# Kernel optimization log

Measured on AMD Instinct MI355X. Metric: run time of the kernel, lower is better.

The kernel has to match this reference:

```python
import jax, jax.numpy as jnp
import numpy as np

SR = 22050.0  # samplerate; nyquist = SR/2


def _conv1d(x, w, b, pad):
    # x: [B, Cin, T], w: [Cout, Cin, K]
    y = jax.lax.conv_general_dilated(x, w, (1,), [(pad, pad)],
                                     dimension_numbers=('NCH', 'OIH', 'NCH'))
    return y + b[None, :, None]


def _lrelu(x):
    return jnp.where(x >= 0, x, 0.2 * x)


def _lin_upsample(x, factor):
    # torch F.upsample(mode='linear', align_corners=False) ~ half-pixel linear resize
    B, C, T = x.shape
    return jax.image.resize(x, (B, C, T * factor), method='linear')


def _oscillator_bank(f, a, sr):
    # f, a: [B, n_osc, T] -> audio [B, T]
    f = jnp.clip(f, 20.0, sr / 2.0)
    phase = jnp.cumsum(f * (2.0 * np.pi / sr), axis=-1)  # cumulative phase integration
    return jnp.sum(jnp.sin(phase) * a, axis=1)


def _noise_bank2(mags, noise):
    # mags: [B, n_coeffs, n_frames] rfft magnitudes per frame; noise: [B, total_samples]
    B, n_coeffs, n_frames = mags.shape
    window = (n_coeffs - 1) * 2
    hop = window // 2
    total = hop * n_frames
    padded = jnp.pad(noise, ((0, 0), (0, hop)))           # [B, total + hop]
    blocks = padded.reshape(B, n_frames + 1, hop)
    frames = jnp.concatenate([blocks[:, :-1], blocks[:, 1:]], axis=-1)  # [B, n_frames, window]
    spec = jnp.fft.rfft(frames, axis=-1)                   # [B, n_frames, n_coeffs]
    spec = spec * mags.transpose(0, 2, 1)                  # filter white noise per frame
    filt = jnp.fft.irfft(spec, n=window, axis=-1)          # (torch normalized rfft/irfft scales cancel)
    out = jnp.zeros((B, hop * (n_frames + 1)), filt.dtype)
    out = out.at[:, :n_frames * hop].add(filt[..., :hop].reshape(B, -1))
    out = out.at[:, hop:].add(filt[..., hop:].reshape(B, -1))
    return out[:, :total].reshape(B, 1, total)


def _forward(x, noise, mw0, mb0, mw1, mb1, mw2, mb2, mw3, mb3, fw, fb,
             gw0, gb0, gw1, gb1, gw2, gb2, gw3, gb3, lw, lb,
             nw0, nb0, nw1, nb1, nw2, nb2, nw3, nb3, nlw, nlb):
    B, _, T = x.shape
    up = noise.shape[1] // T  # upsample_factor = output_size // input_size
    n_osc = fw.shape[0]

    # oscillator frequency ranges (constants, as in __init__)
    stops = np.geomspace(20.0, SR / 2.0, num=n_osc)
    diffs = np.diff(np.concatenate([[0.0], stops]))
    starts = jnp.asarray(stops - diffs, jnp.float32)[None, :, None]
    diffs_j = jnp.asarray(diffs, jnp.float32)[None, :, None]

    # loudness path (main2 -> loudness ** 2)
    h = x
    for w_, b_ in ((gw0, gb0), (gw1, gb1), (gw2, gb2), (gw3, gb3)):
        h = _lrelu(_conv1d(h, w_, b_, 1))
    loud = _conv1d(h, lw, lb, 1) ** 2  # [B, n_osc, T]

    # frequency path (main -> sigmoid -> map to [start, stop])
    h = x
    for w_, b_ in ((mw0, mb0), (mw1, mb1), (mw2, mb2), (mw3, mb3)):
        h = _lrelu(_conv1d(h, w_, b_, 1))
    f = starts + jax.nn.sigmoid(_conv1d(h, fw, fb, 1)) * diffs_j  # [B, n_osc, T]

    h = x
    for w_, b_ in ((nw0, nb0), (nw1, nb1), (nw2, nb2), (nw3, nb3)):
        h = jnp.repeat(h, 2, axis=-1)
        h = _lrelu(_conv1d(h, w_, b_, 3))
    n_l = _conv1d(h, nlw, nlb, 1) ** 2  # [B, 17, 1024]

    loud = _lin_upsample(loud, up)  # [B, n_osc, output_size]
    f = _lin_upsample(f, up)
    harmonic = _oscillator_bank(f, loud, SR).reshape(B, 1, -1)
    return harmonic + _noise_bank2(n_l, noise)


def setup_inputs() -> dict:
    key = jax.random.key(0)
    ks = jax.random.split(key, 40)
    B, Cin, T, c, n_osc, out_size = 16, 128, 64, 512, 128, 16384
    n_coeffs = out_size // 1024 + 1  # 17
    inp = {}
    inp['x'] = jax.random.normal(ks[0], (B, Cin, T), jnp.float32)
    inp['noise'] = jax.random.uniform(ks[1], (B, out_size), jnp.float32, minval=-1.0, maxval=1.0)
    specs = [('mw0', c, Cin, 3), ('mw1', c, c, 3), ('mw2', c, c, 3), ('mw3', c, c, 3), ('fw', n_osc, c, 3),
             ('gw0', c, Cin, 3), ('gw1', c, c, 3), ('gw2', c, c, 3), ('gw3', c, c, 3), ('lw', n_osc, c, 3),
             ('nw0', c, Cin, 7), ('nw1', c, c, 7), ('nw2', c, c, 7), ('nw3', c, c, 7), ('nlw', n_coeffs, c, 3)]
    for j, (nm, o, i, ksz) in enumerate(specs):
        kw, kb = jax.random.split(ks[2 + j])
        inp[nm] = jax.random.normal(kw, (o, i, ksz), jnp.float32) * (1.0 / np.sqrt(i * ksz))
        inp[nm.replace('w', 'b', 1)] = jax.random.normal(kb, (o,), jnp.float32) * 0.01
    return inp


def reference(x, noise, mw0, mb0, mw1, mb1, mw2, mb2, mw3, mb3, fw, fb,
              gw0, gb0, gw1, gb1, gw2, gb2, gw3, gb3, lw, lb,
              nw0, nb0, nw1, nb1, nw2, nb2, nw3, nb3, nlw, nlb):
    return _forward(x, noise, mw0, mb0, mw1, mb1, mw2, mb2, mw3, mb3, fw, fb,
                    gw0, gb0, gw1, gb1, gw2, gb2, gw3, gb3, lw, lb,
                    nw0, nb0, nw1, nb1, nw2, nb2, nw3, nb3, nlw, nlb)
```

## Files before the change

kernel.cpp:

```cpp
#include <hip/hip_runtime.h>
#include <math.h>

#define ACT_LRELU  0
#define ACT_SIGMAP 1
#define ACT_SQUARE 2

typedef __attribute__((ext_vector_type(8))) short v8s;
typedef __attribute__((ext_vector_type(4))) short v4s;
typedef __attribute__((ext_vector_type(16))) float f32x16;

static __device__ __forceinline__ float lrelu(float x) { return x >= 0.f ? x : 0.2f * x; }

static __device__ __forceinline__ short bf16rne(float x) {
  unsigned u = __float_as_uint(x);
  unsigned r = (u + 0x7FFFu + ((u >> 16) & 1u)) >> 16;
  return (short)r;
}
static __device__ __forceinline__ float bf16tof(short h) {
  return __uint_as_float(((unsigned)(unsigned short)h) << 16);
}
static __device__ __forceinline__ void split3(float v, short& h, short& l, short& q) {
  h = bf16rne(v); float r1 = v - bf16tof(h);
  l = bf16rne(r1); float r2 = r1 - bf16tof(l);
  q = bf16rne(r2);
}

__global__ void __launch_bounds__(256) prep_acts(
    const float* __restrict__ x, short* __restrict__ xm3)
{
  int e = blockIdx.x * 256 + threadIdx.x;
  if (e >= 131072) return;
  int b = e >> 13, rem = e & 8191, t = rem >> 7, ci = rem & 127;
  float v = x[((size_t)(b * 128) + ci) * 64 + t];
  short h, l, q; split3(v, h, l, q);
  size_t o = ((size_t)(b * 64) + t) * 128 + ci;
  xm3[0 * 131072 + o] = h;
  xm3[1 * 131072 + o] = l;
  xm3[2 * 131072 + o] = q;
}

__global__ void __launch_bounds__(256) prep_panels(
    const float* mw0, const float* mw1, const float* mw2, const float* mw3, const float* fw,
    const float* gw0, const float* gw1, const float* gw2, const float* gw3, const float* lw,
    short* __restrict__ mP, short* __restrict__ gP)
{
  int i = blockIdx.x * 256 + threadIdx.x;
  const int PER_PATH = 917504;
  if (i >= 2 * PER_PATH) return;
  int path = i >= PER_PATH ? 1 : 0;
  int r = i - path * PER_PATH;
  int layer, Cin, Cout; size_t poff;
  if (r < 65536)       { layer = 0;               Cin = 128; Cout = 512; poff = 0; }
  else if (r < 327680) { layer = 1; r -= 65536;   Cin = 512; Cout = 512; poff = 589824; }
  else if (r < 589824) { layer = 2; r -= 327680;  Cin = 512; Cout = 512; poff = 2949120; }
  else if (r < 851968) { layer = 3; r -= 589824;  Cin = 512; Cout = 512; poff = 5308416; }
  else                 { layer = 4; r -= 851968;  Cin = 512; Cout = 128; poff = 7667712; }
  const float* Wm[5] = {mw0, mw1, mw2, mw3, fw};
  const float* Wg[5] = {gw0, gw1, gw2, gw3, lw};
  const float* W = path ? Wg[layer] : Wm[layer];
  short* P = (path ? gP : mP) + poff;
  int co = r / Cin, ci = r - co * Cin;
  const int K3 = 3 * Cin;
  const float* wp = W + (size_t)(co * Cin + ci) * 3;
#pragma unroll
  for (int tap = 0; tap < 3; ++tap) {
    short h, l, q; split3(wp[tap], h, l, q);
    size_t base = (size_t)co * K3 + tap * Cin + ci;
    P[(size_t)0 * Cout * K3 + base] = h;
    P[(size_t)1 * Cout * K3 + base] = l;
    P[(size_t)2 * Cout * K3 + base] = q;
  }
}

__global__ void __launch_bounds__(256, 2) conv_path(
    const short* __restrict__ actM, const short* __restrict__ actG,
    const short* __restrict__ Pm, const short* __restrict__ Pg,
    const float* __restrict__ BsM, const float* __restrict__ BsG,
    float* __restrict__ foutM, float* __restrict__ foutG,
    short* __restrict__ soutM, short* __restrict__ soutG,
    int Cin, int Cout, int psIn, int psOut, int actMk, int actGk)
{
  const int mtiles = Cout >> 6;
  const int nblk = 2 * mtiles * 16;
  const int Q = nblk >> 3;
  int d = blockIdx.x;
  int idx = (d & 7) * Q + (d >> 3);
  int mt = idx % mtiles;
  int tmp = idx / mtiles;
  int nt = tmp & 15;
  int path = tmp >> 4;

  const short* act = path ? actG : actM;
  const short* P   = path ? Pg : Pm;
  const float* Bs  = path ? BsG : BsM;
  float* fout      = path ? foutG : foutM;
  short* sout      = path ? soutG : soutM;
  const int actk   = path ? actGk : actMk;

  const int K3 = 3 * Cin;
  const int co0 = mt * 64;
  const int n0  = nt * 64;
  const int nci = Cin >> 6;
  const int NT  = 3 * nci;

  const int tid = threadIdx.x;
  const int w = tid >> 6, wm = w & 1, wn = w >> 1;
  const int l = tid & 63;

  __shared__ __align__(16) short Al[3][64 * 72];
  __shared__ __align__(16) short Bl[3][64 * 72];
  __shared__ float bandS[2][128];

  if (actk == ACT_SIGMAP && tid < 128) {
    double lg = log(551.25);
    double stop  = 20.0 * exp(lg * (double)tid / 127.0);
    double start = (tid == 0) ? 0.0 : 20.0 * exp(lg * (double)(tid - 1) / 127.0);
    bandS[0][tid] = (float)start;
    bandS[1][tid] = (float)(stop - start);
  }

  f32x16 acc = {};
  v8s rA[3][2], rB[3][2];

  auto LOADA = [&](int t) {
    int tap = t / nci, ci0 = (t % nci) << 6;
#pragma unroll
    for (int pl = 0; pl < 3; ++pl)
#pragma unroll
      for (int it = 0; it < 2; ++it) {
        int e = it * 256 + tid;
        int row = e >> 3, c8 = e & 7;
        rA[pl][it] = *(const v8s*)&P[(size_t)pl * Cout * K3 + (size_t)(co0 + row) * K3
                                     + tap * Cin + ci0 + c8 * 8];
      }
  };
  auto LOADB = [&](int t) {
    int tap = t / nci, ci0 = (t % nci) << 6;
#pragma unroll
    for (int pl = 0; pl < 3; ++pl)
#pragma unroll
      for (int it = 0; it < 2; ++it) {
        int e = it * 256 + tid;
        int n = e >> 3, c8 = e & 7;
        int gn = n0 + n, bb = gn >> 6, trow = (gn & 63) + tap - 1;
        v8s vv = {};
        if (trow >= 0 && trow < 64)
          vv = *(const v8s*)&act[(size_t)pl * psIn + ((size_t)(bb * 64 + trow)) * Cin
                                 + ci0 + c8 * 8];
        rB[pl][it] = vv;
      }
  };
  auto WRITE = [&]() {
#pragma unroll
    for (int pl = 0; pl < 3; ++pl)
#pragma unroll
      for (int it = 0; it < 2; ++it) {
        int e = it * 256 + tid;
        int row = e >> 3, c8 = e & 7;
        *(v8s*)&Al[pl][row * 72 + c8 * 8] = rA[pl][it];
        *(v8s*)&Bl[pl][row * 72 + c8 * 8] = rB[pl][it];
      }
  };

  LOADA(0); LOADB(0);
  WRITE();
  __syncthreads();

  for (int t = 0; t < NT; ++t) {
    if (t + 1 < NT) { LOADA(t + 1); LOADB(t + 1); }
    const int abase = (wm * 32 + (l & 31)) * 72 + (l >> 5) * 8;
    const int bbase = (wn * 32 + (l & 31)) * 72 + (l >> 5) * 8;
#pragma unroll
    for (int kk = 0; kk < 4; ++kk) {
      v8s a0 = *(const v8s*)&Al[0][abase + kk * 16];
      v8s a1 = *(const v8s*)&Al[1][abase + kk * 16];
      v8s a2 = *(const v8s*)&Al[2][abase + kk * 16];
      v8s b0 = *(const v8s*)&Bl[0][bbase + kk * 16];
      v8s b1 = *(const v8s*)&Bl[1][bbase + kk * 16];
      v8s b2 = *(const v8s*)&Bl[2][bbase + kk * 16];
      acc = __builtin_amdgcn_mfma_f32_32x32x16_bf16(a0, b0, acc, 0, 0, 0);
      acc = __builtin_amdgcn_mfma_f32_32x32x16_bf16(a0, b1, acc, 0, 0, 0);
      acc = __builtin_amdgcn_mfma_f32_32x32x16_bf16(a1, b0, acc, 0, 0, 0);
      acc = __builtin_amdgcn_mfma_f32_32x32x16_bf16(a1, b1, acc, 0, 0, 0);
      acc = __builtin_amdgcn_mfma_f32_32x32x16_bf16(a0, b2, acc, 0, 0, 0);
      acc = __builtin_amdgcn_mfma_f32_32x32x16_bf16(a2, b0, acc, 0, 0, 0);
    }
    __syncthreads();
    if (t + 1 < NT) { WRITE(); __syncthreads(); }
  }

  const int ncol = wn * 32 + (l & 31);
  const int gn = n0 + ncol, bb = gn >> 6, t = gn & 63;
  const int hi4 = 4 * (l >> 5);
#pragma unroll
  for (int q4 = 0; q4 < 4; ++q4) {
    int co = co0 + wm * 32 + q4 * 8 + hi4;
    float4 bia = *(const float4*)&Bs[co];
    const float* bp = &bia.x;
    float z[4];
#pragma unroll
    for (int j = 0; j < 4; ++j) z[j] = acc[q4 * 4 + j] + bp[j];
    if (actk == ACT_LRELU) {
      v4s h4, l4, q4v;
#pragma unroll
      for (int j = 0; j < 4; ++j) {
        float zz = lrelu(z[j]);
        short h, lo, qq; split3(zz, h, lo, qq);
        h4[j] = h; l4[j] = lo; q4v[j] = qq;
      }
      size_t o = ((size_t)(bb * 64) + t) * Cout + co;
      *(v4s*)&sout[0 * (size_t)psOut + o] = h4;
      *(v4s*)&sout[1 * (size_t)psOut + o] = l4;
      *(v4s*)&sout[2 * (size_t)psOut + o] = q4v;
    } else if (actk == ACT_SIGMAP) {
#pragma unroll
      for (int j = 0; j < 4; ++j) {
        float f = bandS[0][co + j] + bandS[1][co + j] / (1.f + expf(-z[j]));
        fout[((size_t)(bb * 128) + co + j) * 64 + t] = f;
      }
    } else {
#pragma unroll
      for (int j = 0; j < 4; ++j)
        fout[((size_t)(bb * 128) + co + j) * 64 + t] = z[j] * z[j];
    }
  }
}

__global__ void __launch_bounds__(256) fold_all(
    const float* __restrict__ nw0, const float* __restrict__ nw1,
    const float* __restrict__ nw2, const float* __restrict__ nw3,
    const float* __restrict__ nlw,
    short* __restrict__ E1, short* __restrict__ E2,
    short* __restrict__ E3, short* __restrict__ E4,
    short* __restrict__ Pnl)
{
  int i = blockIdx.x * 256 + threadIdx.x;
  if (i >= 851968) {
    if (i >= 868352) return;
    int idx = i - 851968;
    int co = idx >> 9, ci = idx & 511;
#pragma unroll
    for (int tap = 0; tap < 3; ++tap) {
      float v = (co < 17) ? nlw[((size_t)(co * 512 + ci)) * 3 + tap] : 0.f;
      short h = bf16rne(v);
      short lo = bf16rne(v - bf16tof(h));
      Pnl[(size_t)(0 * 32 + co) * 1536 + tap * 512 + ci] = h;
      Pnl[(size_t)(1 * 32 + co) * 1536 + tap * 512 + ci] = lo;
    }
    return;
  }
  const float* W; short* Ag; int Cin; int idx;
  if (i < 65536)        { W = nw0; Ag = E1; Cin = 128; idx = i; }
  else if (i < 327680)  { W = nw1; Ag = E2; Cin = 512; idx = i - 65536; }
  else if (i < 589824)  { W = nw2; Ag = E3; Cin = 512; idx = i - 327680; }
  else                  { W = nw3; Ag = E4; Cin = 512; idx = i - 589824; }
  int co = idx / Cin, ci = idx - co * Cin;
  const float* wp = W + (size_t)idx * 7;
  float f[2][4] = {{wp[0],         wp[1] + wp[2], wp[3] + wp[4], wp[5] + wp[6]},
                   {wp[0] + wp[1], wp[2] + wp[3], wp[4] + wp[5], wp[6]}};
  const int K = Cin * 4;
#pragma unroll
  for (int par = 0; par < 2; ++par)
#pragma unroll
    for (int q = 0; q < 4; ++q) {
      float v = f[par][q];
      short h = bf16rne(v);
      short lo = bf16rne(v - bf16tof(h));
      Ag[((size_t)((par * 2 + 0) * 512 + co)) * K + q * Cin + ci] = h;
      Ag[((size_t)((par * 2 + 1) * 512 + co)) * K + q * Cin + ci] = lo;
    }
}

template<int MF, int BNS, int CIN>
__global__ void __launch_bounds__(256, 2) conv_noise(
    const short* __restrict__ actIn, const short* __restrict__ Ag,
    const float* __restrict__ Bs, short* __restrict__ actOut,
    int Sin, int psIn, int psOut)
{
  constexpr int NF   = BNS / 64;
  constexpr int BM   = MF * 64;
  constexpr int AITS = BM / 32;
  constexpr int BITS = BNS / 32;
  constexpr int K    = CIN * 4;
  constexpr int nci  = CIN / 64;
  constexpr int NT   = 4 * nci;
  const int mtiles = 512 / BM;
  const int stiles = Sin / BNS;
  const int nblk = mtiles * 2 * 16 * stiles;
  const int Q = nblk >> 3;
  int d = blockIdx.x;
  int idx = (d & 7) * Q + (d >> 3);
  int mt = idx % mtiles;
  int t1 = idx / mtiles;
  int par = t1 & 1;
  int rest = t1 >> 1;
  int st = rest % stiles;
  int b = rest / stiles;

  const int co0 = mt * BM;
  const int s0 = st * BNS;
  const int soff = par ? -1 : -2;

  const int tid = threadIdx.x;
  const int w = tid >> 6, wm = w & 1, wn = w >> 1;
  const int l = tid & 63;

  __shared__ __align__(16) short Al[2][BM * 72];
  __shared__ __align__(16) short Bl[2][BNS * 72];

  f32x16 acc[MF][NF] = {};
  v8s rA[2][AITS], rB[2][BITS];

  auto LOADA = [&](int t) {
    int q = t / nci, ci0 = (t % nci) << 6;
#pragma unroll
    for (int pl = 0; pl < 2; ++pl)
#pragma unroll
      for (int it = 0; it < AITS; ++it) {
        int e = it * 256 + tid;
        int row = e >> 3, c8 = e & 7;
        rA[pl][it] = *(const v8s*)&Ag[((size_t)((par * 2 + pl) * 512 + co0 + row)) * K
                                      + q * CIN + ci0 + c8 * 8];
      }
  };
  auto LOADB = [&](int t) {
    int q = t / nci, ci0 = (t % nci) << 6;
#pragma unroll
    for (int pl = 0; pl < 2; ++pl)
#pragma unroll
      for (int it = 0; it < BITS; ++it) {
        int e = it * 256 + tid;
        int n = e >> 3, c8 = e & 7;
        int srow = s0 + n + q + soff;
        v8s vv = {};
        if (srow >= 0 && srow < Sin)
          vv = *(const v8s*)&actIn[(size_t)pl * psIn + ((size_t)(b * Sin + srow)) * CIN
                                   + ci0 + c8 * 8];
        rB[pl][it] = vv;
      }
  };
  auto WRITE = [&]() {
#pragma unroll
    for (int pl = 0; pl < 2; ++pl) {
#pragma unroll
      for (int it = 0; it < AITS; ++it) {
        int e = it * 256 + tid;
        *(v8s*)&Al[pl][(e >> 3) * 72 + (e & 7) * 8] = rA[pl][it];
      }
#pragma unroll
      for (int it = 0; it < BITS; ++it) {
        int e = it * 256 + tid;
        *(v8s*)&Bl[pl][(e >> 3) * 72 + (e & 7) * 8] = rB[pl][it];
      }
    }
  };

  LOADA(0); LOADB(0);
  WRITE();
  __syncthreads();

  for (int t = 0; t < NT; ++t) {
    if (t + 1 < NT) { LOADA(t + 1); LOADB(t + 1); }
    const int lr = l & 31, lh = (l >> 5) * 8;
#pragma unroll
    for (int kk = 0; kk < 4; ++kk) {
      v8s ah[MF], al[MF], bh[NF], bl[NF];
#pragma unroll
      for (int fm = 0; fm < MF; ++fm) {
        int ab = (wm * (MF * 32) + fm * 32 + lr) * 72 + kk * 16 + lh;
        ah[fm] = *(const v8s*)&Al[0][ab];
        al[fm] = *(const v8s*)&Al[1][ab];
      }
#pragma unroll
      for (int fn = 0; fn < NF; ++fn) {
        int bb = (wn * (BNS / 2) + fn * 32 + lr) * 72 + kk * 16 + lh;
        bh[fn] = *(const v8s*)&Bl[0][bb];
        bl[fn] = *(const v8s*)&Bl[1][bb];
      }
#pragma unroll
      for (int fm = 0; fm < MF; ++fm)
#pragma unroll
        for (int fn = 0; fn < NF; ++fn) {
          acc[fm][fn] = __builtin_amdgcn_mfma_f32_32x32x16_bf16(ah[fm], bh[fn], acc[fm][fn], 0, 0, 0);
          acc[fm][fn] = __builtin_amdgcn_mfma_f32_32x32x16_bf16(ah[fm], bl[fn], acc[fm][fn], 0, 0, 0);
          acc[fm][fn] = __builtin_amdgcn_mfma_f32_32x32x16_bf16(al[fm], bh[fn], acc[fm][fn], 0, 0, 0);
        }
    }
    __syncthreads();
    if (t + 1 < NT) { WRITE(); __syncthreads(); }
  }

  const int hi4 = 4 * (l >> 5);
  const int T2 = 2 * Sin;
#pragma unroll
  for (int fm = 0; fm < MF; ++fm)
#pragma unroll
    for (int q4 = 0; q4 < 4; ++q4) {
      int co = co0 + wm * (MF * 32) + fm * 32 + q4 * 8 + hi4;
      float4 bia = *(const float4*)&Bs[co];
      const float* bp = &bia.x;
#pragma unroll
      for (int fn = 0; fn < NF; ++fn) {
        int s_l = wn * (BNS / 2) + fn * 32 + (l & 31);
        int t = 2 * (s0 + s_l) + par;
        v4s h4, l4;
#pragma unroll
        for (int j = 0; j < 4; ++j) {
          float z = lrelu(acc[fm][fn][q4 * 4 + j] + bp[j]);
          short h = bf16rne(z);
          h4[j] = h;
          l4[j] = bf16rne(z - bf16tof(h));
        }
        size_t o = ((size_t)(b * T2) + t) * 512 + co;
        *(v4s*)&actOut[0 * (size_t)psOut + o] = h4;
        *(v4s*)&actOut[1 * (size_t)psOut + o] = l4;
      }
    }
}

#define NL_PS4 8388608

__global__ void __launch_bounds__(128) conv_nl_mfma(
    const short* __restrict__ act, const short* __restrict__ Pnl,
    const float* __restrict__ Bs, float* __restrict__ outNl)
{
  const int bid = blockIdx.x;
  const int b = bid >> 4, t0 = (bid & 15) << 6;
  const int tid = threadIdx.x;
  const int w = tid >> 6;
  const int l = tid & 63;

  __shared__ __align__(16) short Al[2 * 3 * 32 * 72];
  __shared__ __align__(16) short Bl[2 * 66 * 72];

  f32x16 acc = {};

  for (int ci0 = 0; ci0 < 512; ci0 += 64) {
    for (int e = tid; e < 1536; e += 128) {
      int c8 = e & 7, row = e >> 3;
      int pl = row >= 96;
      int r2 = row - pl * 96;
      int tap = r2 >> 5, co = r2 & 31;
      v8s vv = *(const v8s*)&Pnl[(size_t)(pl * 32 + co) * 1536 + tap * 512 + ci0 + c8 * 8];
      *(v8s*)&Al[row * 72 + c8 * 8] = vv;
    }
    for (int e = tid; e < 1056; e += 128) {
      int c8 = e & 7, r = (e >> 3) % 66, pl = (e >> 3) / 66;
      int t = t0 + r - 1;
      v8s vv = {};
      if (t >= 0 && t < 1024)
        vv = *(const v8s*)&act[(size_t)pl * NL_PS4 + ((size_t)(b << 10) + t) * 512 + ci0 + c8 * 8];
      *(v8s*)&Bl[(pl * 66 + r) * 72 + c8 * 8] = vv;
    }
    __syncthreads();
    const int lr = l & 31, lh = (l >> 5) * 8;
#pragma unroll
    for (int kk = 0; kk < 4; ++kk)
#pragma unroll
      for (int tap = 0; tap < 3; ++tap) {
        v8s a_h = *(const v8s*)&Al[((0 * 3 + tap) * 32 + lr) * 72 + kk * 16 + lh];
        v8s a_l = *(const v8s*)&Al[((1 * 3 + tap) * 32 + lr) * 72 + kk * 16 + lh];
        int brow = w * 32 + lr + tap;
        v8s b_h = *(const v8s*)&Bl[(0 * 66 + brow) * 72 + kk * 16 + lh];
        v8s b_l = *(const v8s*)&Bl[(1 * 66 + brow) * 72 + kk * 16 + lh];
        acc = __builtin_amdgcn_mfma_f32_32x32x16_bf16(a_h, b_h, acc, 0, 0, 0);
        acc = __builtin_amdgcn_mfma_f32_32x32x16_bf16(a_h, b_l, acc, 0, 0, 0);
        acc = __builtin_amdgcn_mfma_f32_32x32x16_bf16(a_l, b_h, acc, 0, 0, 0);
      }
    __syncthreads();
  }

  const int t = t0 + w * 32 + (l & 31);
  const int hi4 = 4 * (l >> 5);
#pragma unroll
  for (int q4 = 0; q4 < 4; ++q4) {
#pragma unroll
    for (int j = 0; j < 4; ++j) {
      int co = q4 * 8 + hi4 + j;
      if (co < 17) {
        float z = acc[q4 * 4 + j] + Bs[co];
        outNl[((size_t)(b * 17) + co) * 1024 + t] = z * z;
      }
    }
  }
}

__global__ void __launch_bounds__(64) noise_filter(
    const float* __restrict__ noise, const float* __restrict__ mags,
    float* __restrict__ filt)
{
  __shared__ float ct[32], st[32];
  int tid = threadIdx.x;
  if (tid < 32) {
    double a = (double)tid * (3.14159265358979323846 / 16.0);
    ct[tid] = (float)cos(a);
    st[tid] = (float)sin(a);
  }
  __syncthreads();

  int fidx = blockIdx.x * 64 + tid;
  int b = fidx >> 10, i = fidx & 1023;

  float xv[32];
#pragma unroll
  for (int n = 0; n < 32; ++n) {
    int idx = i * 16 + n;
    xv[n] = (idx < 16384) ? noise[(size_t)b * 16384 + idx] : 0.f;
  }

  float Yr[17], Yi[17];
#pragma unroll
  for (int k = 0; k <= 16; ++k) {
    float xr = 0.f, xi = 0.f;
    int kk = 0;
#pragma unroll
    for (int n = 0; n < 32; ++n) {
      xr += xv[n] * ct[kk];
      xi -= xv[n] * st[kk];
      kk = (kk + k) & 31;
    }
    float m = mags[((size_t)b * 17 + k) * 1024 + i];
    Yr[k] = xr * m;
    Yi[k] = xi * m;
  }

  float* fo = filt + ((size_t)b * 1024 + i) * 32;
#pragma unroll
  for (int n = 0; n < 32; ++n) {
    float v = Yr[0] + ((n & 1) ? -Yr[16] : Yr[16]);
    int kk = n;
#pragma unroll
    for (int k = 1; k <= 15; ++k) {
      v += 2.f * (Yr[k] * ct[kk] - Yi[k] * st[kk]);
      kk = (kk + n) & 31;
    }
    fo[n] = v * (1.f / 32.f);
  }
}

static __device__ __forceinline__ int clamp64(int i) { return i < 0 ? 0 : (i > 63 ? 63 : i); }

__global__ void __launch_bounds__(256) osc_phase(
    const float* __restrict__ fsm, double* __restrict__ phaseBase)
{
  const int o = blockIdx.x, b = blockIdx.y;
  const float* frow = fsm + (size_t)(b * 128 + o) * 64;
  const int c = threadIdx.x;

  const float ic0 = ((float)(c * 64) - 127.5f) * (1.0f / 256.0f);
  const int ilo = (int)floorf(ic0);
  float f0 = frow[clamp64(ilo)], f1 = frow[clamp64(ilo + 1)], f2 = frow[clamp64(ilo + 2)];

  double local = 0.0;
#pragma unroll 8
  for (int j = 0; j < 64; ++j) {
    float ic = ic0 + (float)j * (1.0f / 256.0f);
    float fl = floorf(ic);
    float w  = ic - fl;
    bool hi = ((int)fl) > ilo;
    float fa = hi ? f1 : f0;
    float fb = hi ? f2 : f1;
    float f = fa * (1.f - w) + fb * w;
    f = fminf(fmaxf(f, 20.f), 11025.f);
    local += (double)f;
  }
  local *= (1.0 / 22050.0);

  __shared__ double ps[256];
  ps[c] = local;
  __syncthreads();
  for (int off = 1; off < 256; off <<= 1) {
    double v = (c >= off) ? ps[c - off] : 0.0;
    __syncthreads();
    ps[c] += v;
    __syncthreads();
  }
  phaseBase[(size_t)(b * 128 + o) * 256 + c] = ps[c] - local;
}

__global__ void __launch_bounds__(128) osc_sum(
    const float* __restrict__ fsm, const float* __restrict__ lsm,
    const double* __restrict__ phaseBase, const float* __restrict__ filt,
    float* __restrict__ out)
{
  const int c = blockIdx.x, b = blockIdx.y;
  const int tid = threadIdx.x;
  __shared__ float contrib[128][65];
  __shared__ float part[2][64];
  const int o = tid;
  const float* frow = fsm + (size_t)(b * 128 + o) * 64;
  const float* arow = lsm + (size_t)(b * 128 + o) * 64;

  double pb = phaseBase[(size_t)(b * 128 + o) * 256 + c];
  float fb0 = (float)(pb - floor(pb));

  const float ic0 = ((float)(c * 64) - 127.5f) * (1.0f / 256.0f);
  const int ilo = (int)floorf(ic0);
  float f0 = frow[clamp64(ilo)], f1 = frow[clamp64(ilo + 1)], f2 = frow[clamp64(ilo + 2)];
  float a0 = arow[clamp64(ilo)], a1 = arow[clamp64(ilo + 1)], a2 = arow[clamp64(ilo + 2)];

  float rel = 0.f, comp = 0.f;
#pragma unroll 8
  for (int j = 0; j < 64; ++j) {
    float ic = ic0 + (float)j * (1.0f / 256.0f);
    float fl = floorf(ic);
    float w  = ic - fl;
    bool hi = ((int)fl) > ilo;
    float fa = hi ? f1 : f0;
    float fb = hi ? f2 : f1;
    float f = fa * (1.f - w) + fb * w;
    f = fminf(fmaxf(f, 20.f), 11025.f);
    float y = f * (1.0f / 22050.0f) - comp;
    float t = rel + y;
    comp = (t - rel) - y;
    rel = t;
    float tot = fb0 + rel;
    float frac = tot - floorf(tot);
    float s = sinpif(2.f * frac);
    float aa = hi ? a1 : a0;
    float ab = hi ? a2 : a1;
    float am = aa * (1.f - w) + ab * w;
    contrib[o][j] = s * am;
  }
  __syncthreads();
  int half = tid >> 6, tl = tid & 63;
  float sum = 0.f;
  for (int oo = 0; oo < 64; ++oo) sum += contrib[half * 64 + oo][tl];
  part[half][tl] = sum;
  __syncthreads();
  if (tid < 64) {
    int t = c * 64 + tid;
    float v = part[0][tid] + part[1][tid];
    int i0 = t >> 4, r = t & 15;
    v += filt[((size_t)(b << 10) + i0) * 32 + r];
    if (i0 > 0) v += filt[((size_t)(b << 10) + i0 - 1) * 32 + 16 + r];
    out[(size_t)b * 16384 + t] = v;
  }
}

extern "C" void kernel_launch(void* const* d_in, const int* in_sizes, int n_in,
                              void* d_out, int out_size, void* d_ws, size_t ws_size,
                              hipStream_t stream)
{
  (void)in_sizes; (void)n_in; (void)out_size; (void)ws_size;

  const float* x     = (const float*)d_in[0];
  const float* noise = (const float*)d_in[1];
  const float* mw0 = (const float*)d_in[2];  const float* mb0 = (const float*)d_in[3];
  const float* mw1 = (const float*)d_in[4];  const float* mb1 = (const float*)d_in[5];
  const float* mw2 = (const float*)d_in[6];  const float* mb2 = (const float*)d_in[7];
  const float* mw3 = (const float*)d_in[8];  const float* mb3 = (const float*)d_in[9];
  const float* fw  = (const float*)d_in[10]; const float* fb  = (const float*)d_in[11];
  const float* gw0 = (const float*)d_in[12]; const float* gb0 = (const float*)d_in[13];
  const float* gw1 = (const float*)d_in[14]; const float* gb1 = (const float*)d_in[15];
  const float* gw2 = (const float*)d_in[16]; const float* gb2 = (const float*)d_in[17];
  const float* gw3 = (const float*)d_in[18]; const float* gb3 = (const float*)d_in[19];
  const float* lw  = (const float*)d_in[20]; const float* lb  = (const float*)d_in[21];
  const float* nw0 = (const float*)d_in[22]; const float* nb0 = (const float*)d_in[23];
  const float* nw1 = (const float*)d_in[24]; const float* nb1 = (const float*)d_in[25];
  const float* nw2 = (const float*)d_in[26]; const float* nb2 = (const float*)d_in[27];
  const float* nw3 = (const float*)d_in[28]; const float* nb3 = (const float*)d_in[29];
  const float* nlw = (const float*)d_in[30]; const float* nlb = (const float*)d_in[31];

  char* W8 = (char*)d_ws;
  short* mP  = (short*)(W8 + 0);
  short* gP  = (short*)(W8 + 16515072);
  short* hm0 = (short*)(W8 + 33030144);
  short* hm1 = (short*)(W8 + 36175872);
  short* hg0 = (short*)(W8 + 39321600);
  short* hg1 = (short*)(W8 + 42467328);
  short* xm3 = (short*)(W8 + 58720256);
  float* fsm = (float*)(W8 + 59506688);
  float* lsm = (float*)(W8 + 60030976);
  short* Pnl = (short*)(W8 + 60555264);

  short* E4  = (short*)(W8 + 0);
  short* E3  = (short*)(W8 + 33554432);
  short* E2  = (short*)(W8 + 41943040);
  short* E1  = (short*)(W8 + 50331648);
  short* l1out = (short*)(W8 + 52428800);
  short* l2out = (short*)(W8 + 25165824);
  short* l3out = (short*)(W8 + 8388608);
  short* l4act = (short*)(W8 + 25165824);

  float* nl   = (float*)(W8 + 0);
  float* filt = (float*)(W8 + 1114112);
  double* phaseBase = (double*)(W8 + 4194304);

  float* out = (float*)d_out;

  const int PS_X = 131072;
  const int PS_H = 524288;

  prep_acts<<<512, 256, 0, stream>>>(x, xm3);
  prep_panels<<<7168, 256, 0, stream>>>(mw0, mw1, mw2, mw3, fw,
                                        gw0, gw1, gw2, gw3, lw, mP, gP);

  conv_path<<<256, 256, 0, stream>>>(xm3, xm3, mP + 0, gP + 0, mb0, gb0,
      nullptr, nullptr, hm0, hg0, 128, 512, PS_X, PS_H, ACT_LRELU, ACT_LRELU);
  conv_path<<<256, 256, 0, stream>>>(hm0, hg0, mP + 589824, gP + 589824, mb1, gb1,
      nullptr, nullptr, hm1, hg1, 512, 512, PS_H, PS_H, ACT_LRELU, ACT_LRELU);
  conv_path<<<256, 256, 0, stream>>>(hm1, hg1, mP + 2949120, gP + 2949120, mb2, gb2,
      nullptr, nullptr, hm0, hg0, 512, 512, PS_H, PS_H, ACT_LRELU, ACT_LRELU);
  conv_path<<<256, 256, 0, stream>>>(hm0, hg0, mP + 5308416, gP + 5308416, mb3, gb3,
      nullptr, nullptr, hm1, hg1, 512, 512, PS_H, PS_H, ACT_LRELU, ACT_LRELU);
  conv_path<<<64, 256, 0, stream>>>(hm1, hg1, mP + 7667712, gP + 7667712, fb, lb,
      fsm, lsm, nullptr, nullptr, 512, 128, PS_H, 0, ACT_SIGMAP, ACT_SQUARE);

  fold_all<<<3392, 256, 0, stream>>>(nw0, nw1, nw2, nw3, nlw, E1, E2, E3, E4, Pnl);
  conv_noise<1, 64, 128><<<256, 256, 0, stream>>>(xm3, E1, nb0, l1out, 64, PS_X, 1048576);
  conv_noise<2, 64, 512><<<256, 256, 0, stream>>>(l1out, E2, nb1, l2out, 128, 1048576, 2097152);
  conv_noise<2, 128, 512><<<256, 256, 0, stream>>>(l2out, E3, nb2, l3out, 256, 2097152, 4194304);
  conv_noise<2, 128, 512><<<512, 256, 0, stream>>>(l3out, E4, nb3, l4act, 512, 4194304, 8388608);

  conv_nl_mfma<<<256, 128, 0, stream>>>(l4act, Pnl, nlb, nl);

  noise_filter<<<256, 64, 0, stream>>>(noise, nl, filt);

  osc_phase<<<dim3(128, 16), 256, 0, stream>>>(fsm, phaseBase);
  osc_sum<<<dim3(256, 16), 128, 0, stream>>>(fsm, lsm, phaseBase, filt, out);
}
```

Baseline: 553.2 us.

## Split conv path GEMMs across taps with partial sums and separate finalize kernels

Each conv layer of the two MLP-like paths is now split by kernel tap into independent blocks (three times as many blocks, 128 threads each, with a smaller K tile). Each block writes fp32 partial sums, and a new finalize kernel adds the three taps, applies bias and the activation, and re-splits the result into bf16 planes. The gain path also drops to two bf16 planes, which cuts its MFMA work. The aim is more parallelism and occupancy across the GPU. The cost is extra global traffic for the partial buffers, extra launches, and lower precision on the gain path.

```diff
diff --git a/kernel.cpp b/kernel.cpp
--- a/kernel.cpp
+++ b/kernel.cpp
@@ -72,157 +72,195 @@
   }
 }
 
-__global__ void __launch_bounds__(256, 2) conv_path(
+__global__ void __launch_bounds__(128, 2) conv_path_tap(
     const short* __restrict__ actM, const short* __restrict__ actG,
     const short* __restrict__ Pm, const short* __restrict__ Pg,
-    const float* __restrict__ BsM, const float* __restrict__ BsG,
-    float* __restrict__ foutM, float* __restrict__ foutG,
-    short* __restrict__ soutM, short* __restrict__ soutG,
-    int Cin, int Cout, int psIn, int psOut, int actMk, int actGk)
+    float* __restrict__ partial, int Cin, int Cout, int psIn)
 {
   const int mtiles = Cout >> 6;
-  const int nblk = 2 * mtiles * 16;
+  const int nblk = 2 * mtiles * 16 * 3;
   const int Q = nblk >> 3;
   int d = blockIdx.x;
   int idx = (d & 7) * Q + (d >> 3);
-  int mt = idx % mtiles;
-  int tmp = idx / mtiles;
-  int nt = tmp & 15;
-  int path = tmp >> 4;
+  int mt = idx % mtiles; int r = idx / mtiles;
+  int nt = r & 15; r >>= 4;
+  int tap = r % 3; int path = r / 3;
 
   const short* act = path ? actG : actM;
   const short* P   = path ? Pg : Pm;
-  const float* Bs  = path ? BsG : BsM;
-  float* fout      = path ? foutG : foutM;
-  short* sout      = path ? soutG : soutM;
-  const int actk   = path ? actGk : actMk;
-
   const int K3 = 3 * Cin;
   const int co0 = mt * 64;
-  const int n0  = nt * 64;
-  const int nci = Cin >> 6;
-  const int NT  = 3 * nci;
+  const int NT  = Cin >> 5;
+  const int npl = path ? 2 : 3;
 
   const int tid = threadIdx.x;
-  const int w = tid >> 6, wm = w & 1, wn = w >> 1;
+  const int w = tid >> 6;
   const int l = tid & 63;
 
-  __shared__ __align__(16) short Al[3][64 * 72];
-  __shared__ __align__(16) short Bl[3][64 * 72];
+  __shared__ __align__(16) short Al[3][64 * 40];
+  __shared__ __align__(16) short Bl[3][64 * 40];
+
+  f32x16 acc[2] = {};
+  v8s rA[3][2], rB[3][2];
+
+  auto LOADA = [&](int t) {
+    int ci0 = t << 5;
+#pragma unroll
+    for (int pl = 0; pl < 3; ++pl) {
+      if (pl >= npl) break;
+#pragma unroll
+      for (int it = 0; it < 2; ++it) {
+        int e = it * 128 + tid;
+        int row = e >> 2, c8 = e & 3;
+        rA[pl][it] = *(const v8s*)&P[(size_t)pl * Cout * K3 + (size_t)(co0 + row) * K3
+                                     + tap * Cin + ci0 + c8 * 8];
+      }
+    }
+  };
+  auto LOADB = [&](int t) {
+    int ci0 = t << 5;
+#pragma unroll
+    for (int pl = 0; pl < 3; ++pl) {
+      if (pl >= npl) break;
+#pragma unroll
+      for (int it = 0; it < 2; ++it) {
+        int e = it * 128 + tid;
+        int n = e >> 2, c8 = e & 3;
+        int trow = n + tap - 1;
+        v8s vv = {};
+        if (trow >= 0 && trow < 64)
+          vv = *(const v8s*)&act[(size_t)pl * psIn + ((size_t)(nt * 64 + trow)) * Cin
+                                 + ci0 + c8 * 8];
+        rB[pl][it] = vv;
+      }
+    }
+  };
+  auto WRITE = [&]() {
+#pragma unroll
+    for (int pl = 0; pl < 3; ++pl) {
+      if (pl >= npl) break;
+#pragma unroll
+      for (int it = 0; it < 2; ++it) {
+        int e = it * 128 + tid;
+        *(v8s*)&Al[pl][(e >> 2) * 40 + (e & 3) * 8] = rA[pl][it];
+        *(v8s*)&Bl[pl][(e >> 2) * 40 + (e & 3) * 8] = rB[pl][it];
+      }
+    }
+  };
+
+  LOADA(0); LOADB(0);
+  WRITE();
+  __syncthreads();
+
+  for (int t = 0; t < NT; ++t) {
+    if (t + 1 < NT) { LOADA(t + 1); LOADB(t + 1); }
+    const int lr = l & 31, lh = (l >> 5) * 8;
+#pragma unroll
+    for (int kk = 0; kk < 2; ++kk) {
+      const int ao = (w * 32 + lr) * 40 + kk * 16 + lh;
+      v8s a0 = *(const v8s*)&Al[0][ao];
+      v8s a1 = *(const v8s*)&Al[1][ao];
+#pragma unroll
+      for (int fn = 0; fn < 2; ++fn) {
+        const int bo = (fn * 32 + lr) * 40 + kk * 16 + lh;
+        v8s b0 = *(const v8s*)&Bl[0][bo];
+        v8s b1 = *(const v8s*)&Bl[1][bo];
+        acc[fn] = __builtin_amdgcn_mfma_f32_32x32x16_bf16(a0, b0, acc[fn], 0, 0, 0);
+        acc[fn] = __builtin_amdgcn_mfma_f32_32x32x16_bf16(a0, b1, acc[fn], 0, 0, 0);
+        acc[fn] = __builtin_amdgcn_mfma_f32_32x32x16_bf16(a1, b0, acc[fn], 0, 0, 0);
+        if (path == 0) {
+          v8s a2 = *(const v8s*)&Al[2][ao];
+          v8s b2 = *(const v8s*)&Bl[2][bo];
+          acc[fn] = __builtin_amdgcn_mfma_f32_32x32x16_bf16(a1, b1, acc[fn], 0, 0, 0);
+          acc[fn] = __builtin_amdgcn_mfma_f32_32x32x16_bf16(a0, b2, acc[fn], 0, 0, 0);
+          acc[fn] = __builtin_amdgcn_mfma_f32_32x32x16_bf16(a2, b0, acc[fn], 0, 0, 0);
+        }
+      }
+    }
+    __syncthreads();
+    if (t + 1 < NT) { WRITE(); __syncthreads(); }
+  }
+
+  const int hi4 = 4 * (l >> 5);
+  const size_t pbase = (size_t)(tap * 2 + path) * 1024;
+#pragma unroll
+  for (int fn = 0; fn < 2; ++fn) {
+    int gn = nt * 64 + fn * 32 + (l & 31);
+#pragma unroll
+    for (int q4 = 0; q4 < 4; ++q4) {
+      int co = co0 + w * 32 + q4 * 8 + hi4;
+      float4 v = {acc[fn][q4 * 4 + 0], acc[fn][q4 * 4 + 1],
+                  acc[fn][q4 * 4 + 2], acc[fn][q4 * 4 + 3]};
+      *(float4*)&partial[(pbase + gn) * Cout + co] = v;
+    }
+  }
+}
+
+__global__ void __launch_bounds__(256) finalize_lrelu(
+    const float* __restrict__ partial,
+    const float* __restrict__ BsM, const float* __restrict__ BsG,
+    short* __restrict__ soutM, short* __restrict__ soutG)
+{
+  int e = blockIdx.x * 256 + threadIdx.x;
+  int c4 = e & 127, gn = (e >> 7) & 1023, path = e >> 17;
+  const float* Bs = path ? BsG : BsM;
+  short* sout = path ? soutG : soutM;
+  size_t base = ((size_t)(path) * 1024 + gn) * 512 + c4 * 4;
+  const size_t TS = (size_t)2 * 1024 * 512;
+  float4 s0 = *(const float4*)&partial[base];
+  float4 s1 = *(const float4*)&partial[base + TS];
+  float4 s2 = *(const float4*)&partial[base + 2 * TS];
+  float4 bi = *(const float4*)&Bs[c4 * 4];
+  const float* p0 = &s0.x; const float* p1 = &s1.x;
+  const float* p2 = &s2.x; const float* pb = &bi.x;
+  v4s h4, l4, q4v;
+#pragma unroll
+  for (int j = 0; j < 4; ++j) {
+    float z = lrelu(p0[j] + p1[j] + p2[j] + pb[j]);
+    short h, lo, qq; split3(z, h, lo, qq);
+    h4[j] = h; l4[j] = lo; q4v[j] = qq;
+  }
+  size_t o = (size_t)gn * 512 + c4 * 4;
+  *(v4s*)&sout[0 * 524288 + o] = h4;
+  *(v4s*)&sout[1 * 524288 + o] = l4;
+  *(v4s*)&sout[2 * 524288 + o] = q4v;
+}
+
+__global__ void __launch_bounds__(256) finalize_l5(
+    const float* __restrict__ partial,
+    const float* __restrict__ fb, const float* __restrict__ lb,
+    float* __restrict__ fsm, float* __restrict__ lsm)
+{
   __shared__ float bandS[2][128];
-
-  if (actk == ACT_SIGMAP && tid < 128) {
+  int tid = threadIdx.x;
+  if (tid < 128) {
     double lg = log(551.25);
     double stop  = 20.0 * exp(lg * (double)tid / 127.0);
     double start = (tid == 0) ? 0.0 : 20.0 * exp(lg * (double)(tid - 1) / 127.0);
     bandS[0][tid] = (float)start;
     bandS[1][tid] = (float)(stop - start);
   }
-
-  f32x16 acc = {};
-  v8s rA[3][2], rB[3][2];
-
-  auto LOADA = [&](int t) {
-    int tap = t / nci, ci0 = (t % nci) << 6;
-#pragma unroll
-    for (int pl = 0; pl < 3; ++pl)
-#pragma unroll
-      for (int it = 0; it < 2; ++it) {
-        int e = it * 256 + tid;
-        int row = e >> 3, c8 = e & 7;
-        rA[pl][it] = *(const v8s*)&P[(size_t)pl * Cout * K3 + (size_t)(co0 + row) * K3
-                                     + tap * Cin + ci0 + c8 * 8];
-      }
-  };
-  auto LOADB = [&](int t) {
-    int tap = t / nci, ci0 = (t % nci) << 6;
-#pragma unroll
-    for (int pl = 0; pl < 3; ++pl)
-#pragma unroll
-      for (int it = 0; it < 2; ++it) {
-        int e = it * 256 + tid;
-        int n = e >> 3, c8 = e & 7;
-        int gn = n0 + n, bb = gn >> 6, trow = (gn & 63) + tap - 1;
-        v8s vv = {};
-        if (trow >= 0 && trow < 64)
-          vv = *(const v8s*)&act[(size_t)pl * psIn + ((size_t)(bb * 64 + trow)) * Cin
-                                 + ci0 + c8 * 8];
-        rB[pl][it] = vv;
-      }
-  };
-  auto WRITE = [&]() {
-#pragma unroll
-    for (int pl = 0; pl < 3; ++pl)
-#pragma unroll
-      for (int it = 0; it < 2; ++it) {
-        int e = it * 256 + tid;
-        int row = e >> 3, c8 = e & 7;
-        *(v8s*)&Al[pl][row * 72 + c8 * 8] = rA[pl][it];
-        *(v8s*)&Bl[pl][row * 72 + c8 * 8] = rB[pl][it];
-      }
-  };
-
-  LOADA(0); LOADB(0);
-  WRITE();
   __syncthreads();
 
-  for (int t = 0; t < NT; ++t) {
-    if (t + 1 < NT) { LOADA(t + 1); LOADB(t + 1); }
-    const int abase = (wm * 32 + (l & 31)) * 72 + (l >> 5) * 8;
-    const int bbase = (wn * 32 + (l & 31)) * 72 + (l >> 5) * 8;
-#pragma unroll
-    for (int kk = 0; kk < 4; ++kk) {
-      v8s a0 = *(const v8s*)&Al[0][abase + kk * 16];
-      v8s a1 = *(const v8s*)&Al[1][abase + kk * 16];
-      v8s a2 = *(const v8s*)&Al[2][abase + kk * 16];
-      v8s b0 = *(const v8s*)&Bl[0][bbase + kk * 16];
-      v8s b1 = *(const v8s*)&Bl[1][bbase + kk * 16];
-      v8s b2 = *(const v8s*)&Bl[2][bbase + kk * 16];
-      acc = __builtin_amdgcn_mfma_f32_32x32x16_bf16(a0, b0, acc, 0, 0, 0);
-      acc = __builtin_amdgcn_mfma_f32_32x32x16_bf16(a0, b1, acc, 0, 0, 0);
-      acc = __builtin_amdgcn_mfma_f32_32x32x16_bf16(a1, b0, acc, 0, 0, 0);
-      acc = __builtin_amdgcn_mfma_f32_32x32x16_bf16(a1, b1, acc, 0, 0, 0);
-      acc = __builtin_amdgcn_mfma_f32_32x32x16_bf16(a0, b2, acc, 0, 0, 0);
-      acc = __builtin_amdgcn_mfma_f32_32x32x16_bf16(a2, b0, acc, 0, 0, 0);
-    }
-    __syncthreads();
-    if (t + 1 < NT) { WRITE(); __syncthreads(); }
-  }
-
-  const int ncol = wn * 32 + (l & 31);
-  const int gn = n0 + ncol, bb = gn >> 6, t = gn & 63;
-  const int hi4 = 4 * (l >> 5);
-#pragma unroll
-  for (int q4 = 0; q4 < 4; ++q4) {
-    int co = co0 + wm * 32 + q4 * 8 + hi4;
-    float4 bia = *(const float4*)&Bs[co];
-    const float* bp = &bia.x;
-    float z[4];
-#pragma unroll
-    for (int j = 0; j < 4; ++j) z[j] = acc[q4 * 4 + j] + bp[j];
-    if (actk == ACT_LRELU) {
-      v4s h4, l4, q4v;
-#pragma unroll
-      for (int j = 0; j < 4; ++j) {
-        float zz = lrelu(z[j]);
-        short h, lo, qq; split3(zz, h, lo, qq);
-        h4[j] = h; l4[j] = lo; q4v[j] = qq;
-      }
-      size_t o = ((size_t)(bb * 64) + t) * Cout + co;
-      *(v4s*)&sout[0 * (size_t)psOut + o] = h4;
-      *(v4s*)&sout[1 * (size_t)psOut + o] = l4;
-      *(v4s*)&sout[2 * (size_t)psOut + o] = q4v;
-    } else if (actk == ACT_SIGMAP) {
-#pragma unroll
-      for (int j = 0; j < 4; ++j) {
-        float f = bandS[0][co + j] + bandS[1][co + j] / (1.f + expf(-z[j]));
-        fout[((size_t)(bb * 128) + co + j) * 64 + t] = f;
-      }
-    } else {
-#pragma unroll
-      for (int j = 0; j < 4; ++j)
-        fout[((size_t)(bb * 128) + co + j) * 64 + t] = z[j] * z[j];
-    }
+  int e = blockIdx.x * 256 + tid;
+  int c4 = e & 31, gn = (e >> 5) & 1023, path = e >> 15;
+  size_t base = ((size_t)(path) * 1024 + gn) * 128 + c4 * 4;
+  const size_t TS = (size_t)2 * 1024 * 128;
+  float4 s0 = *(const float4*)&partial[base];
+  float4 s1 = *(const float4*)&partial[base + TS];
+  float4 s2 = *(const float4*)&partial[base + 2 * TS];
+  float4 bi = *(const float4*)&((path ? lb : fb)[c4 * 4]);
+  const float* p0 = &s0.x; const float* p1 = &s1.x;
+  const float* p2 = &s2.x; const float* pb = &bi.x;
+  int b = gn >> 6, t = gn & 63;
+#pragma unroll
+  for (int j = 0; j < 4; ++j) {
+    int co = c4 * 4 + j;
+    float z = p0[j] + p1[j] + p2[j] + pb[j];
+    if (path == 0)
+      fsm[((size_t)(b * 128) + co) * 64 + t] = bandS[0][co] + bandS[1][co] / (1.f + expf(-z));
+    else
+      lsm[((size_t)(b * 128) + co) * 64 + t] = z * z;
   }
 }
 
@@ -669,6 +707,7 @@
   short* hm1 = (short*)(W8 + 36175872);
   short* hg0 = (short*)(W8 + 39321600);
   short* hg1 = (short*)(W8 + 42467328);
+  float* partial = (float*)(W8 + 45613056);
   short* xm3 = (short*)(W8 + 58720256);
   float* fsm = (float*)(W8 + 59506688);
   float* lsm = (float*)(W8 + 60030976);
@@ -696,16 +735,16 @@
   prep_panels<<<7168, 256, 0, stream>>>(mw0, mw1, mw2, mw3, fw,
                                         gw0, gw1, gw2, gw3, lw, mP, gP);
 
-  conv_path<<<256, 256, 0, stream>>>(xm3, xm3, mP + 0, gP + 0, mb0, gb0,
-      nullptr, nullptr, hm0, hg0, 128, 512, PS_X, PS_H, ACT_LRELU, ACT_LRELU);
-  conv_path<<<256, 256, 0, stream>>>(hm0, hg0, mP + 589824, gP + 589824, mb1, gb1,
-      nullptr, nullptr, hm1, hg1, 512, 512, PS_H, PS_H, ACT_LRELU, ACT_LRELU);
-  conv_path<<<256, 256, 0, stream>>>(hm1, hg1, mP + 2949120, gP + 2949120, mb2, gb2,
-      nullptr, nullptr, hm0, hg0, 512, 512, PS_H, PS_H, ACT_LRELU, ACT_LRELU);
-  conv_path<<<256, 256, 0, stream>>>(hm0, hg0, mP + 5308416, gP + 5308416, mb3, gb3,
-      nullptr, nullptr, hm1, hg1, 512, 512, PS_H, PS_H, ACT_LRELU, ACT_LRELU);
-  conv_path<<<64, 256, 0, stream>>>(hm1, hg1, mP + 7667712, gP + 7667712, fb, lb,
-      fsm, lsm, nullptr, nullptr, 512, 128, PS_H, 0, ACT_SIGMAP, ACT_SQUARE);
+  conv_path_tap<<<768, 128, 0, stream>>>(xm3, xm3, mP + 0, gP + 0, partial, 128, 512, PS_X);
+  finalize_lrelu<<<1024, 256, 0, stream>>>(partial, mb0, gb0, hm0, hg0);
+  conv_path_tap<<<768, 128, 0, stream>>>(hm0, hg0, mP + 589824, gP + 589824, partial, 512, 512, PS_H);
+  finalize_lrelu<<<1024, 256, 0, stream>>>(partial, mb1, gb1, hm1, hg1);
+  conv_path_tap<<<768, 128, 0, stream>>>(hm1, hg1, mP + 2949120, gP + 2949120, partial, 512, 512, PS_H);
+  finalize_lrelu<<<1024, 256, 0, stream>>>(partial, mb2, gb2, hm0, hg0);
+  conv_path_tap<<<768, 128, 0, stream>>>(hm0, hg0, mP + 5308416, gP + 5308416, partial, 512, 512, PS_H);
+  finalize_lrelu<<<1024, 256, 0, stream>>>(partial, mb3, gb3, hm1, hg1);
+  conv_path_tap<<<192, 128, 0, stream>>>(hm1, hg1, mP + 7667712, gP + 7667712, partial, 512, 128, PS_H);
+  finalize_l5<<<256, 256, 0, stream>>>(partial, fb, lb, fsm, lsm);
 
   fold_all<<<3392, 256, 0, stream>>>(nw0, nw1, nw2, nw3, nlw, E1, E2, E3, E4, Pnl);
   conv_noise<1, 64, 128><<<256, 256, 0, stream>>>(xm3, E1, nb0, l1out, 64, PS_X, 1048576);
```

Result: no change. 554.7 us (+0.3%).
